# Kernel optimization log

Hardware: AMD Instinct MI355X
Metric: run time of the kernel (lower is better)

The kernel has to match this reference:

```python
import jax, jax.numpy as jnp
import numpy as np

DIMS = 2048
HEAD_DIM = 64
NUM_HEADS = DIMS // HEAD_DIM   # 32
GQA_HEADS = 2                  # KV heads
EPS = 1e-8


def setup_inputs() -> dict:
    key = jax.random.key(0)
    ks = jax.random.split(key, 6)
    b, s = 2, 2048
    kv_dims = HEAD_DIM * GQA_HEADS  # 128
    x = jax.random.normal(ks[0], (b, s, DIMS), dtype=jnp.float32)
    Wq = jax.random.normal(ks[1], (DIMS, DIMS), dtype=jnp.float32) * 0.02
    Wk = jax.random.normal(ks[2], (kv_dims, DIMS), dtype=jnp.float32) * 0.02
    Wv = jax.random.normal(ks[3], (kv_dims, DIMS), dtype=jnp.float32) * 0.02
    Wo = jax.random.normal(ks[4], (DIMS, DIMS), dtype=jnp.float32) * 0.02
    norm_scale = jnp.ones((DIMS,), dtype=jnp.float32)           # RMSNorm.scale
    split_scale = jnp.full((DIMS,), 0.1, dtype=jnp.float32)     # RMS_split.scale
    return {"x": x, "norm_scale": norm_scale, "split_scale": split_scale,
            "Wq": Wq, "Wk": Wk, "Wv": Wv, "Wo": Wo}


def reference(x, norm_scale, split_scale, Wq, Wk, Wv, Wo):
    b, s, d = x.shape
    H, G, dh = NUM_HEADS, GQA_HEADS, HEAD_DIM
    hpg = H // G  # query heads per KV group

    # RMS_split pre-norm: RMSNorm (l2-norm based) then elementwise scale
    nrm = jnp.linalg.norm(x, axis=-1, keepdims=True) * (d ** -0.5)
    h = (norm_scale * x / (nrm + EPS)) * split_scale

    # projections (nn.Linear with weight [out, in], no bias)
    q = (h @ Wq.T).reshape(b, s, H, dh)          # b s H dh
    k = (h @ Wk.T).reshape(b, s, G, dh)          # b s G dh
    v = (h @ Wv.T).reshape(b, s, G, dh)

    # group query heads: b G hpg s dh
    q = q.transpose(0, 2, 1, 3).reshape(b, G, hpg, s, dh)
    k = k.transpose(0, 2, 1, 3)                  # b G s dh
    v = v.transpose(0, 2, 1, 3)                  # b G s dh

    scores = jnp.einsum('bghsd,bgtd->bghst', q, k) / np.float32(np.sqrt(dh))
    attn = jax.nn.softmax(scores, axis=-1)
    out = jnp.einsum('bghst,bgtd->bghsd', attn, v)   # b G hpg s dh

    out = out.reshape(b, H, s, dh).transpose(0, 2, 1, 3).reshape(b, s, H * dh)
    return x + out @ Wo.T
```

## Files before the change

kernel.cpp:

```cpp
#include <hip/hip_runtime.h>

typedef unsigned short u16;
typedef unsigned int u32;
typedef __bf16 bf16x8 __attribute__((ext_vector_type(8)));
typedef float f32x4 __attribute__((ext_vector_type(4)));

#define DIMS 2048
#define SEQ 2048
#define BATCH 2
#define NH 32
#define NG 2
#define DH 64
#define MROWS (BATCH * SEQ)
#define KVD (NG * DH)

#define SCL2 (0.125f * 1.44269504088896f)

__device__ __forceinline__ u16 f2bf(float f) {
  u32 u = __float_as_uint(f);
  u32 r = u + 0x7fffu + ((u >> 16) & 1u);
  return (u16)(r >> 16);
}
__device__ __forceinline__ u32 pack2(float a, float b) {
  return (u32)f2bf(a) | ((u32)f2bf(b) << 16);
}
__device__ __forceinline__ void glds16(const u16* g, u16* l) {
  __builtin_amdgcn_global_load_lds(
      (const __attribute__((address_space(1))) void*)g,
      (__attribute__((address_space(3))) void*)l, 16, 0, 0);
}

__global__ __launch_bounds__(256) void rms_split_kernel(
    const float* __restrict__ x, const float* __restrict__ ns,
    const float* __restrict__ ss, u16* __restrict__ h) {
  const int row = blockIdx.x;
  const int tid = threadIdx.x;
  const float* xr = x + (size_t)row * DIMS;
  float4 v0 = ((const float4*)xr)[tid];
  float4 v1 = ((const float4*)xr)[tid + 256];
  float s = v0.x * v0.x + v0.y * v0.y + v0.z * v0.z + v0.w * v0.w +
            v1.x * v1.x + v1.y * v1.y + v1.z * v1.z + v1.w * v1.w;
#pragma unroll
  for (int d = 1; d < 64; d <<= 1) s += __shfl_xor(s, d, 64);
  __shared__ float red[4];
  if ((tid & 63) == 0) red[tid >> 6] = s;
  __syncthreads();
  float tot = red[0] + red[1] + red[2] + red[3];
  float inv = 1.0f / (sqrtf(tot * (1.0f / DIMS)) + 1e-8f);
  float4 a0 = ((const float4*)ns)[tid];
  float4 a1 = ((const float4*)ns)[tid + 256];
  float4 b0 = ((const float4*)ss)[tid];
  float4 b1 = ((const float4*)ss)[tid + 256];
  uint2 o0, o1;
  o0.x = pack2(v0.x * a0.x * b0.x * inv, v0.y * a0.y * b0.y * inv);
  o0.y = pack2(v0.z * a0.z * b0.z * inv, v0.w * a0.w * b0.w * inv);
  o1.x = pack2(v1.x * a1.x * b1.x * inv, v1.y * a1.y * b1.y * inv);
  o1.y = pack2(v1.z * a1.z * b1.z * inv, v1.w * a1.w * b1.w * inv);
  uint2* hr = (uint2*)(h + (size_t)row * DIMS);
  hr[tid] = o0;
  hr[tid + 256] = o1;
}

__global__ __launch_bounds__(256) void cvt_kernel(const float* __restrict__ w,
                                                  u16* __restrict__ o) {
  const int i = blockIdx.x * 256 + threadIdx.x;
  float4 v = ((const float4*)w)[i];
  uint2 r;
  r.x = pack2(v.x, v.y);
  r.y = pack2(v.z, v.w);
  ((uint2*)o)[i] = r;
}

template <int OUTF>
__global__ __launch_bounds__(256) void gemm_bt(
    const u16* __restrict__ A, const u16* __restrict__ B, void* __restrict__ Cv,
    const float* __restrict__ R, int M, int N, int K) {
  __shared__ u16 As[128 * 32];
  __shared__ u16 Bs[128 * 32];
  const int tid = threadIdx.x;
  const int lane = tid & 63;
  const int wv = tid >> 6;
  const int fr = lane & 15;
  const int fq = lane >> 4;
  const int m0 = blockIdx.y * 128;
  const int n0 = blockIdx.x * 128;
  const int wm = wv & 1;
  const int wn = wv >> 1;

  const int srow = tid >> 2;
  const int scol = (tid & 3) * 8;
  const u16* Ag0 = A + (size_t)(m0 + srow) * K + scol;
  const u16* Ag1 = A + (size_t)(m0 + srow + 64) * K + scol;
  const u16* Bg0 = B + (size_t)(n0 + srow) * K + scol;
  const u16* Bg1 = B + (size_t)(n0 + srow + 64) * K + scol;
  u16* Al0 = As + wv * 512;
  u16* Al1 = As + 2048 + wv * 512;
  u16* Bl0 = Bs + wv * 512;
  u16* Bl1 = Bs + 2048 + wv * 512;

  f32x4 acc[4][4];
#pragma unroll
  for (int i = 0; i < 4; ++i)
#pragma unroll
    for (int j = 0; j < 4; ++j)
#pragma unroll
      for (int e = 0; e < 4; ++e) acc[i][j][e] = 0.0f;

  const u16* ap[4];
  const u16* bp[4];
#pragma unroll
  for (int i = 0; i < 4; ++i) {
    ap[i] = As + (wm * 64 + i * 16 + fr) * 32 + fq * 8;
    bp[i] = Bs + (wn * 64 + i * 16 + fr) * 32 + fq * 8;
  }

  for (int k0 = 0; k0 < K; k0 += 32) {
    glds16(Ag0 + k0, Al0);
    glds16(Ag1 + k0, Al1);
    glds16(Bg0 + k0, Bl0);
    glds16(Bg1 + k0, Bl1);
    __syncthreads();
    bf16x8 af[4], bf[4];
#pragma unroll
    for (int i = 0; i < 4; ++i) {
      af[i] = *(const bf16x8*)ap[i];
      bf[i] = *(const bf16x8*)bp[i];
    }
#pragma unroll
    for (int i = 0; i < 4; ++i)
#pragma unroll
      for (int j = 0; j < 4; ++j)
        acc[i][j] = __builtin_amdgcn_mfma_f32_16x16x32_bf16(af[i], bf[j],
                                                            acc[i][j], 0, 0, 0);
    __syncthreads();
  }

#pragma unroll
  for (int i = 0; i < 4; ++i) {
    const int m = m0 + wm * 64 + i * 16 + fq * 4;
#pragma unroll
    for (int j = 0; j < 4; ++j) {
      const int n = n0 + wn * 64 + j * 16 + fr;
#pragma unroll
      for (int r = 0; r < 4; ++r) {
        const size_t idx = (size_t)(m + r) * N + n;
        if (OUTF == 0)
          ((u16*)Cv)[idx] = f2bf(acc[i][j][r]);
        else
          ((float*)Cv)[idx] = R[idx] + acc[i][j][r];
      }
    }
  }
}

__global__ __launch_bounds__(256) void gemm_kv(
    const u16* __restrict__ h, const u16* __restrict__ Wk,
    const u16* __restrict__ Wv, u16* __restrict__ kb, u16* __restrict__ vtb) {
  __shared__ u16 As[32 * 32];
  __shared__ u16 Bs[128 * 32];
  const int tid = threadIdx.x;
  const int lane = tid & 63;
  const int wv = tid >> 6;
  const int fr = lane & 15;
  const int fq = lane >> 4;
  const int m0 = blockIdx.x * 32;
  const int l4 = lane >> 2;
  const int lc = (lane & 3) * 8;
  const u16* B = blockIdx.z ? Wv : Wk;

  f32x4 acc[2][2];
#pragma unroll
  for (int i = 0; i < 2; ++i)
#pragma unroll
    for (int j = 0; j < 2; ++j)
#pragma unroll
      for (int e = 0; e < 4; ++e) acc[i][j][e] = 0.0f;

  for (int k0 = 0; k0 < DIMS; k0 += 32) {
#pragma unroll
    for (int s = 0; s < 2; ++s) {
      const int c = wv * 2 + s;
      glds16(B + (size_t)(c * 16 + l4) * DIMS + k0 + lc, Bs + c * 512);
    }
    if (wv < 2)
      glds16(h + (size_t)(m0 + wv * 16 + l4) * DIMS + k0 + lc, As + wv * 512);
    __syncthreads();
    bf16x8 a0 = *(const bf16x8*)(As + (fr)*32 + fq * 8);
    bf16x8 a1 = *(const bf16x8*)(As + (16 + fr) * 32 + fq * 8);
    bf16x8 b0 = *(const bf16x8*)(Bs + (wv * 32 + fr) * 32 + fq * 8);
    bf16x8 b1 = *(const bf16x8*)(Bs + (wv * 32 + 16 + fr) * 32 + fq * 8);
    acc[0][0] = __builtin_amdgcn_mfma_f32_16x16x32_bf16(a0, b0, acc[0][0], 0, 0, 0);
    acc[0][1] = __builtin_amdgcn_mfma_f32_16x16x32_bf16(a0, b1, acc[0][1], 0, 0, 0);
    acc[1][0] = __builtin_amdgcn_mfma_f32_16x16x32_bf16(a1, b0, acc[1][0], 0, 0, 0);
    acc[1][1] = __builtin_amdgcn_mfma_f32_16x16x32_bf16(a1, b1, acc[1][1], 0, 0, 0);
    __syncthreads();
  }

#pragma unroll
  for (int mi = 0; mi < 2; ++mi)
#pragma unroll
    for (int ni = 0; ni < 2; ++ni)
#pragma unroll
      for (int r = 0; r < 4; ++r) {
        const int m = m0 + mi * 16 + fq * 4 + r;
        const int n = wv * 32 + ni * 16 + fr;
        if (blockIdx.z)
          vtb[(size_t)n * MROWS + m] = f2bf(acc[mi][ni][r]);
        else
          kb[(size_t)m * KVD + n] = f2bf(acc[mi][ni][r]);
      }
}

__global__ __launch_bounds__(256, 4) void attn_kernel(
    const u16* __restrict__ q, const u16* __restrict__ kbuf,
    const u16* __restrict__ vT, u16* __restrict__ out) {
  __shared__ u16 Ks[2 * 64 * 32];
  __shared__ u16 Vs[2 * 64 * 32];
  __shared__ u16 Ps[128 * 72];
  const int tid = threadIdx.x;
  const int lane = tid & 63;
  const int wv = tid >> 6;
  const int fr = lane & 15;
  const int fq = lane >> 4;
  const int b = blockIdx.x >> 5;
  const int hq = blockIdx.x & 31;
  const int g = hq >> 4;
  const int q0 = blockIdx.y * 128;
  const int l4 = lane >> 2;
  const int lc = (lane & 3) * 8;

  bf16x8 af[2][2];
#pragma unroll
  for (int mt = 0; mt < 2; ++mt)
#pragma unroll
    for (int kx = 0; kx < 2; ++kx)
      af[mt][kx] = *(const bf16x8*)(q +
                                    (size_t)(b * SEQ + q0 + wv * 32 + mt * 16 +
                                             fr) *
                                        DIMS +
                                    hq * DH + kx * 32 + fq * 8);

  f32x4 Oa[2][4];
  float lacc[2][4];
#pragma unroll
  for (int mt = 0; mt < 2; ++mt)
#pragma unroll
    for (int r = 0; r < 4; ++r) {
      lacc[mt][r] = 0.0f;
#pragma unroll
      for (int e = 0; e < 4; ++e) Oa[mt][r][e] = 0.0f;
    }

  for (int t0 = 0; t0 < SEQ; t0 += 64) {
    if (wv < 2) {
#pragma unroll
      for (int s = 0; s < 4; ++s)
        glds16(kbuf + (size_t)(b * SEQ + t0 + s * 16 + l4) * KVD + g * DH +
                   wv * 32 + lc,
               Ks + (wv * 4 + s) * 512);
    } else {
#pragma unroll
      for (int s = 0; s < 4; ++s)
        glds16(vT + (size_t)(g * DH + s * 16 + l4) * MROWS + b * SEQ + t0 +
                   (wv - 2) * 32 + lc,
               Vs + ((wv - 2) * 4 + s) * 512);
    }
    __syncthreads();

#pragma unroll
    for (int nt = 0; nt < 4; ++nt) {
      bf16x8 b0 = *(const bf16x8*)(Ks + (nt * 16 + fr) * 32 + fq * 8);
      bf16x8 b1 = *(const bf16x8*)(Ks + 2048 + (nt * 16 + fr) * 32 + fq * 8);
      f32x4 s0, s1;
#pragma unroll
      for (int e = 0; e < 4; ++e) { s0[e] = 0.0f; s1[e] = 0.0f; }
      s0 = __builtin_amdgcn_mfma_f32_16x16x32_bf16(af[0][0], b0, s0, 0, 0, 0);
      s0 = __builtin_amdgcn_mfma_f32_16x16x32_bf16(af[0][1], b1, s0, 0, 0, 0);
      s1 = __builtin_amdgcn_mfma_f32_16x16x32_bf16(af[1][0], b0, s1, 0, 0, 0);
      s1 = __builtin_amdgcn_mfma_f32_16x16x32_bf16(af[1][1], b1, s1, 0, 0, 0);
#pragma unroll
      for (int r = 0; r < 4; ++r) {
        const float p0 = __builtin_amdgcn_exp2f(s0[r] * SCL2);
        const float p1 = __builtin_amdgcn_exp2f(s1[r] * SCL2);
        lacc[0][r] += p0;
        lacc[1][r] += p1;
        Ps[(wv * 32 + fq * 4 + r) * 72 + nt * 16 + fr] = f2bf(p0);
        Ps[(wv * 32 + 16 + fq * 4 + r) * 72 + nt * 16 + fr] = f2bf(p1);
      }
    }

#pragma unroll
    for (int kx = 0; kx < 2; ++kx) {
      bf16x8 p0 = *(const bf16x8*)(Ps + (wv * 32 + fr) * 72 + kx * 32 + fq * 8);
      bf16x8 p1 =
          *(const bf16x8*)(Ps + (wv * 32 + 16 + fr) * 72 + kx * 32 + fq * 8);
#pragma unroll
      for (int j = 0; j < 4; ++j) {
        bf16x8 vf =
            *(const bf16x8*)(Vs + kx * 2048 + (j * 16 + fr) * 32 + fq * 8);
        Oa[0][j] =
            __builtin_amdgcn_mfma_f32_16x16x32_bf16(p0, vf, Oa[0][j], 0, 0, 0);
        Oa[1][j] =
            __builtin_amdgcn_mfma_f32_16x16x32_bf16(p1, vf, Oa[1][j], 0, 0, 0);
      }
    }
    __syncthreads();
  }

#pragma unroll
  for (int mt = 0; mt < 2; ++mt)
#pragma unroll
    for (int r = 0; r < 4; ++r) {
#pragma unroll
      for (int d = 1; d < 16; d <<= 1)
        lacc[mt][r] += __shfl_xor(lacc[mt][r], d, 64);
      const float invl = 1.0f / lacc[mt][r];
      const int row = q0 + wv * 32 + mt * 16 + fq * 4 + r;
#pragma unroll
      for (int j = 0; j < 4; ++j)
        out[(size_t)(b * SEQ + row) * DIMS + hq * DH + j * 16 + fr] =
            f2bf(Oa[mt][j][r] * invl);
    }
}

extern "C" void kernel_launch(void* const* d_in, const int* in_sizes, int n_in,
                              void* d_out, int out_size, void* d_ws,
                              size_t ws_size, hipStream_t stream) {
  const float* x = (const float*)d_in[0];
  const float* ns = (const float*)d_in[1];
  const float* ssc = (const float*)d_in[2];
  const float* Wq = (const float*)d_in[3];
  const float* Wk = (const float*)d_in[4];
  const float* Wv = (const float*)d_in[5];
  const float* Wo = (const float*)d_in[6];

  char* ws = (char*)d_ws;
  u16* hbuf = (u16*)(ws);
  u16* bWq = (u16*)(ws + 16777216);
  u16* bWk = (u16*)(ws + 25165824);
  u16* bWv = (u16*)(ws + 25690112);
  u16* bWo = (u16*)(ws + 26214400);
  u16* qb = (u16*)(ws + 34603008);
  u16* kb = (u16*)(ws + 51380224);
  u16* vtb = (u16*)(ws + 52428800);
  u16* ab = (u16*)(ws + 53477376);

  rms_split_kernel<<<dim3(4096), dim3(256), 0, stream>>>(x, ns, ssc, hbuf);
  cvt_kernel<<<dim3(4096), dim3(256), 0, stream>>>(Wq, bWq);
  cvt_kernel<<<dim3(256), dim3(256), 0, stream>>>(Wk, bWk);
  cvt_kernel<<<dim3(256), dim3(256), 0, stream>>>(Wv, bWv);
  cvt_kernel<<<dim3(4096), dim3(256), 0, stream>>>(Wo, bWo);

  gemm_bt<0><<<dim3(16, 32), dim3(256), 0, stream>>>(hbuf, bWq, qb, nullptr,
                                                     4096, 2048, 2048);
  gemm_kv<<<dim3(128, 1, 2), dim3(256), 0, stream>>>(hbuf, bWk, bWv, kb, vtb);
  attn_kernel<<<dim3(64, 16), dim3(256), 0, stream>>>(qb, kb, vtb, ab);
  gemm_bt<1><<<dim3(16, 32), dim3(256), 0, stream>>>(ab, bWo, d_out, x, 4096,
                                                     2048, 2048);
}
```

Baseline: 359.4 us.

## Keep attention probabilities in registers via transposed S and 16x16x16 MFMA

Computes the score tile transposed (K as the A operand, Q as B) so each lane's exp'd scores already match the A-operand layout of a 16x16x16 bf16 MFMA. P can then feed the PV product straight from registers, dropping the Ps LDS round trip. K/V tiles are reloaded into a new LDS layout, row sums are reduced by cross-lane shuffles, and the final normalizer is fetched with a shuffle. In exchange, PV uses the older K=16 MFMA, which needs twice as many instructions, and this relies on the bf16_1k builtin or an inline-asm fallback.

```diff
diff --git a/kernel.cpp b/kernel.cpp
--- a/kernel.cpp
+++ b/kernel.cpp
@@ -4,6 +4,7 @@
 typedef unsigned int u32;
 typedef __bf16 bf16x8 __attribute__((ext_vector_type(8)));
 typedef float f32x4 __attribute__((ext_vector_type(4)));
+typedef short s16x4 __attribute__((ext_vector_type(4)));
 
 #define DIMS 2048
 #define SEQ 2048
@@ -28,6 +29,14 @@
   __builtin_amdgcn_global_load_lds(
       (const __attribute__((address_space(1))) void*)g,
       (__attribute__((address_space(3))) void*)l, 16, 0, 0);
+}
+__device__ __forceinline__ f32x4 mfma16(s16x4 a, s16x4 b, f32x4 c) {
+#if __has_builtin(__builtin_amdgcn_mfma_f32_16x16x16bf16_1k)
+  return __builtin_amdgcn_mfma_f32_16x16x16bf16_1k(a, b, c, 0, 0, 0);
+#else
+  asm("v_mfma_f32_16x16x16_bf16 %0, %1, %2, %0" : "+v"(c) : "v"(a), "v"(b));
+  return c;
+#endif
 }
 
 __global__ __launch_bounds__(256) void rms_split_kernel(
@@ -214,9 +223,8 @@
 __global__ __launch_bounds__(256, 4) void attn_kernel(
     const u16* __restrict__ q, const u16* __restrict__ kbuf,
     const u16* __restrict__ vT, u16* __restrict__ out) {
-  __shared__ u16 Ks[2 * 64 * 32];
-  __shared__ u16 Vs[2 * 64 * 32];
-  __shared__ u16 Ps[128 * 72];
+  __shared__ u16 Ks[8 * 512];
+  __shared__ u16 Vs[8 * 512];
   const int tid = threadIdx.x;
   const int lane = tid & 63;
   const int wv = tid >> 6;
@@ -226,8 +234,6 @@
   const int hq = blockIdx.x & 31;
   const int g = hq >> 4;
   const int q0 = blockIdx.y * 128;
-  const int l4 = lane >> 2;
-  const int lc = (lane & 3) * 8;
 
   bf16x8 af[2][2];
 #pragma unroll
@@ -241,80 +247,72 @@
                                     hq * DH + kx * 32 + fq * 8);
 
   f32x4 Oa[2][4];
-  float lacc[2][4];
+  float lacc[2] = {0.0f, 0.0f};
 #pragma unroll
   for (int mt = 0; mt < 2; ++mt)
 #pragma unroll
+    for (int j = 0; j < 4; ++j)
+#pragma unroll
+      for (int e = 0; e < 4; ++e) Oa[mt][j][e] = 0.0f;
+
+  const u16* ksrc = kbuf + (size_t)(b * SEQ + lane) * KVD + g * DH;
+  const u16* vsrc = vT + (size_t)(g * DH + lane) * MROWS + b * SEQ;
+
+  for (int t0 = 0; t0 < SEQ; t0 += 64) {
+#pragma unroll
+    for (int s = 0; s < 2; ++s) {
+      const int c = wv * 2 + s;
+      glds16(ksrc + (size_t)t0 * KVD + (c >> 2) * 32 + (c & 3) * 8,
+             Ks + c * 512);
+      glds16(vsrc + t0 + c * 8, Vs + c * 512);
+    }
+    __syncthreads();
+
+#pragma unroll
+    for (int nt = 0; nt < 4; ++nt) {
+      bf16x8 k0 = *(const bf16x8*)(Ks + fq * 512 + (nt * 16 + fr) * 8);
+      bf16x8 k1 = *(const bf16x8*)(Ks + (4 + fq) * 512 + (nt * 16 + fr) * 8);
+      s16x4 vf[4];
+#pragma unroll
+      for (int j = 0; j < 4; ++j)
+        vf[j] = *(const s16x4*)(Vs + (nt * 2 + (fq >> 1)) * 512 +
+                                (j * 16 + fr) * 8 + (fq & 1) * 4);
+#pragma unroll
+      for (int mt = 0; mt < 2; ++mt) {
+        f32x4 sa = {0.0f, 0.0f, 0.0f, 0.0f};
+        sa = __builtin_amdgcn_mfma_f32_16x16x32_bf16(k0, af[mt][0], sa, 0, 0, 0);
+        sa = __builtin_amdgcn_mfma_f32_16x16x32_bf16(k1, af[mt][1], sa, 0, 0, 0);
+        const float p0 = __builtin_amdgcn_exp2f(sa[0] * SCL2);
+        const float p1 = __builtin_amdgcn_exp2f(sa[1] * SCL2);
+        const float p2 = __builtin_amdgcn_exp2f(sa[2] * SCL2);
+        const float p3 = __builtin_amdgcn_exp2f(sa[3] * SCL2);
+        lacc[mt] += (p0 + p1) + (p2 + p3);
+        union {
+          s16x4 v;
+          u32 u[2];
+        } pu;
+        pu.u[0] = pack2(p0, p1);
+        pu.u[1] = pack2(p2, p3);
+#pragma unroll
+        for (int j = 0; j < 4; ++j)
+          Oa[mt][j] = mfma16(pu.v, vf[j], Oa[mt][j]);
+      }
+    }
+    __syncthreads();
+  }
+
+#pragma unroll
+  for (int mt = 0; mt < 2; ++mt) {
+    float l = lacc[mt];
+    l += __shfl_xor(l, 16, 64);
+    l += __shfl_xor(l, 32, 64);
+    lacc[mt] = l;
+  }
+#pragma unroll
+  for (int mt = 0; mt < 2; ++mt)
+#pragma unroll
     for (int r = 0; r < 4; ++r) {
-      lacc[mt][r] = 0.0f;
-#pragma unroll
-      for (int e = 0; e < 4; ++e) Oa[mt][r][e] = 0.0f;
-    }
-
-  for (int t0 = 0; t0 < SEQ; t0 += 64) {
-    if (wv < 2) {
-#pragma unroll
-      for (int s = 0; s < 4; ++s)
-        glds16(kbuf + (size_t)(b * SEQ + t0 + s * 16 + l4) * KVD + g * DH +
-                   wv * 32 + lc,
-               Ks + (wv * 4 + s) * 512);
-    } else {
-#pragma unroll
-      for (int s = 0; s < 4; ++s)
-        glds16(vT + (size_t)(g * DH + s * 16 + l4) * MROWS + b * SEQ + t0 +
-                   (wv - 2) * 32 + lc,
-               Vs + ((wv - 2) * 4 + s) * 512);
-    }
-    __syncthreads();
-
-#pragma unroll
-    for (int nt = 0; nt < 4; ++nt) {
-      bf16x8 b0 = *(const bf16x8*)(Ks + (nt * 16 + fr) * 32 + fq * 8);
-      bf16x8 b1 = *(const bf16x8*)(Ks + 2048 + (nt * 16 + fr) * 32 + fq * 8);
-      f32x4 s0, s1;
-#pragma unroll
-      for (int e = 0; e < 4; ++e) { s0[e] = 0.0f; s1[e] = 0.0f; }
-      s0 = __builtin_amdgcn_mfma_f32_16x16x32_bf16(af[0][0], b0, s0, 0, 0, 0);
-      s0 = __builtin_amdgcn_mfma_f32_16x16x32_bf16(af[0][1], b1, s0, 0, 0, 0);
-      s1 = __builtin_amdgcn_mfma_f32_16x16x32_bf16(af[1][0], b0, s1, 0, 0, 0);
-      s1 = __builtin_amdgcn_mfma_f32_16x16x32_bf16(af[1][1], b1, s1, 0, 0, 0);
-#pragma unroll
-      for (int r = 0; r < 4; ++r) {
-        const float p0 = __builtin_amdgcn_exp2f(s0[r] * SCL2);
-        const float p1 = __builtin_amdgcn_exp2f(s1[r] * SCL2);
-        lacc[0][r] += p0;
-        lacc[1][r] += p1;
-        Ps[(wv * 32 + fq * 4 + r) * 72 + nt * 16 + fr] = f2bf(p0);
-        Ps[(wv * 32 + 16 + fq * 4 + r) * 72 + nt * 16 + fr] = f2bf(p1);
-      }
-    }
-
-#pragma unroll
-    for (int kx = 0; kx < 2; ++kx) {
-      bf16x8 p0 = *(const bf16x8*)(Ps + (wv * 32 + fr) * 72 + kx * 32 + fq * 8);
-      bf16x8 p1 =
-          *(const bf16x8*)(Ps + (wv * 32 + 16 + fr) * 72 + kx * 32 + fq * 8);
-#pragma unroll
-      for (int j = 0; j < 4; ++j) {
-        bf16x8 vf =
-            *(const bf16x8*)(Vs + kx * 2048 + (j * 16 + fr) * 32 + fq * 8);
-        Oa[0][j] =
-            __builtin_amdgcn_mfma_f32_16x16x32_bf16(p0, vf, Oa[0][j], 0, 0, 0);
-        Oa[1][j] =
-            __builtin_amdgcn_mfma_f32_16x16x32_bf16(p1, vf, Oa[1][j], 0, 0, 0);
-      }
-    }
-    __syncthreads();
-  }
-
-#pragma unroll
-  for (int mt = 0; mt < 2; ++mt)
-#pragma unroll
-    for (int r = 0; r < 4; ++r) {
-#pragma unroll
-      for (int d = 1; d < 16; d <<= 1)
-        lacc[mt][r] += __shfl_xor(lacc[mt][r], d, 64);
-      const float invl = 1.0f / lacc[mt][r];
+      const float invl = 1.0f / __shfl(lacc[mt], fq * 4 + r, 64);
       const int row = q0 + wv * 32 + mt * 16 + fq * 4 + r;
 #pragma unroll
       for (int j = 0; j < 4; ++j)
```

Result: slower. 369.2 us (+2.7%).
